# Optimization experiments

Hardware: AMD Instinct MI355X
Metric: run time of the kernel (lower is better)

Reference implementation:

```python
import jax, jax.numpy as jnp
import numpy as np

DIM = 1024
H = 16
HD = DIM // H  # 64
K = 256


def setup_inputs() -> dict:
    key = jax.random.key(0)
    ks = jax.random.split(key, 8)
    x = jax.random.normal(ks[0], (4, 4096, DIM), dtype=jnp.float32)
    # torch nn.Linear weights are (out, in); y = x @ W.T
    Wq = jax.random.normal(ks[1], (DIM, DIM), dtype=jnp.float32) * (DIM ** -0.5)
    Wk = jax.random.normal(ks[2], (DIM, DIM), dtype=jnp.float32) * (DIM ** -0.5)
    Wv = jax.random.normal(ks[3], (DIM, DIM), dtype=jnp.float32) * (DIM ** -0.5)
    E = jax.random.normal(ks[4], (K, HD), dtype=jnp.float32)
    F = jax.random.normal(ks[5], (K, HD), dtype=jnp.float32)
    Wo = jax.random.normal(ks[6], (DIM, DIM), dtype=jnp.float32) * (DIM ** -0.5)
    bo = jax.random.normal(ks[7], (DIM,), dtype=jnp.float32) * 0.01
    return {"x": x, "Wq": Wq, "Wk": Wk, "Wv": Wv, "E": E, "F": F, "Wo": Wo, "bo": bo}


def reference(x, Wq, Wk, Wv, E, F, Wo, bo):
    B, N, D = x.shape
    d = HD
    q = (x @ Wq.T).reshape(B, N, H, d).transpose(0, 2, 1, 3)  # (B,H,N,d)
    k = (x @ Wk.T).reshape(B, N, H, d).transpose(0, 2, 1, 3)
    v = (x @ Wv.T).reshape(B, N, H, d).transpose(0, 2, 1, 3)
    # Faithful to source: einsum contracts over n (sequence), elementwise in d.
    k_proj = jnp.einsum('bhnd,kd->bhkd', k, E)  # (B,H,K,d)
    v_proj = jnp.einsum('bhnd,kd->bhkd', v, F)
    attn = jnp.einsum('bhnd,bhkd->bhnk', q, k_proj) / (d ** 0.5)  # (B,H,N,K)
    attn = jax.nn.softmax(attn, axis=-1)
    out = jnp.einsum('bhnk,bhkd->bhnd', attn, v_proj)
    out = out.transpose(0, 2, 1, 3).reshape(B, N, D)
    return out @ Wo.T + bo
```

## Files before the change

### kernel.cpp

```cpp
#include <hip/hip_runtime.h>

#define DIM 1024
#define BATCH 4
#define SEQ 4096
#define NH 16
#define HD 64
#define KP 256

typedef float f32x4 __attribute__((ext_vector_type(4)));
typedef _Float16 half8 __attribute__((ext_vector_type(8)));

__device__ __forceinline__ void gll16(const void* g, void* l) {
  __builtin_amdgcn_global_load_lds(
      (const __attribute__((address_space(1))) void*)g,
      (__attribute__((address_space(3))) void*)l, 16, 0, 0);
}

#define DPPF(v, ctrl)                                                        \
  __builtin_bit_cast(float, __builtin_amdgcn_mov_dpp(                        \
                                __builtin_bit_cast(int, v), ctrl, 0xF, 0xF, true))

__global__ void k_cvt(const float* __restrict__ s, _Float16* __restrict__ d) {
  int i = (blockIdx.x * 256 + threadIdx.x) * 8;
  f32x4 a = *(const f32x4*)(s + i);
  f32x4 b = *(const f32x4*)(s + i + 4);
  half8 h;
  h[0] = a[0]; h[1] = a[1]; h[2] = a[2]; h[3] = a[3];
  h[4] = b[0]; h[5] = b[1]; h[6] = b[2]; h[7] = b[3];
  *(half8*)(d + i) = h;
}

__global__ void k_cvtw(const float* __restrict__ Wq, const float* __restrict__ Wo,
                       _Float16* __restrict__ Wq_h, _Float16* __restrict__ Wo_h) {
  int bb = blockIdx.x;
  const float* s = (bb < 512) ? Wq : Wo;
  _Float16* d = (bb < 512) ? Wq_h : Wo_h;
  int i = ((bb & 511) * 256 + threadIdx.x) * 8;
  f32x4 a = *(const f32x4*)(s + i);
  f32x4 b = *(const f32x4*)(s + i + 4);
  half8 h;
  h[0] = a[0]; h[1] = a[1]; h[2] = a[2]; h[3] = a[3];
  h[4] = b[0]; h[5] = b[1]; h[6] = b[2]; h[7] = b[3];
  *(half8*)(d + i) = h;
}

__global__ void k_misc(const float* __restrict__ E, const float* __restrict__ F,
                       _Float16* __restrict__ E_h, _Float16* __restrict__ Ft,
                       float* __restrict__ xsum) {
  int bb = blockIdx.x;
  if (bb < 16) {
    xsum[bb * 256 + threadIdx.x] = 0.f;
  } else if (bb < 24) {
    int i = ((bb - 16) * 256 + threadIdx.x) * 8;
    f32x4 a = *(const f32x4*)(E + i);
    f32x4 b = *(const f32x4*)(E + i + 4);
    half8 h;
    h[0] = a[0]; h[1] = a[1]; h[2] = a[2]; h[3] = a[3];
    h[4] = b[0]; h[5] = b[1]; h[6] = b[2]; h[7] = b[3];
    *(half8*)(E_h + i) = h;
  } else {
    int i = (bb - 24) * 256 + threadIdx.x;
    int k = i >> 6, d = i & 63;
    Ft[d * KP + (k & 15) * 16 + (k >> 4)] = (_Float16)F[i];
  }
}

__global__ void k_xsum(const _Float16* __restrict__ xh, float* __restrict__ xs) {
  int c = blockIdx.x * 256 + threadIdx.x;
  int b = blockIdx.y;
  int n0 = blockIdx.z * 128;
  const _Float16* p = xh + (size_t)(b * SEQ + n0) * DIM + c;
  float s = 0.f;
  #pragma unroll 8
  for (int i = 0; i < 128; i++) s += (float)p[i * DIM];
  atomicAdd(&xs[b * DIM + c], s);
}

__global__ void k_sksv(const float* __restrict__ xs, const float* __restrict__ Wk,
                       const float* __restrict__ Wv, float* __restrict__ Sk,
                       float* __restrict__ Sv) {
  int idx = blockIdx.x * 4 + (threadIdx.x >> 6);
  int lane = threadIdx.x & 63;
  int kv = idx >> 12;
  int rem = idx & 4095;
  int b = rem >> 10, c = rem & 1023;
  const float* W = (kv ? Wv : Wk) + c * DIM;
  const float* xp = xs + b * DIM;
  float a = 0.f;
  #pragma unroll
  for (int i = 0; i < 16; i++) a += xp[lane + i * 64] * W[lane + i * 64];
  for (int off = 32; off; off >>= 1) a += __shfl_down(a, off);
  if (lane == 0) (kv ? Sv : Sk)[rem] = a;
}

template <int MODE>
__global__ __launch_bounds__(512, 2) void k_gemm(const _Float16* __restrict__ A,
                                                 const _Float16* __restrict__ Bw,
                                                 void* __restrict__ Cout,
                                                 const float* __restrict__ sb) {
  __shared__ _Float16 sh[4][2][8192];
  const int tid = threadIdx.x;
  const int w = tid >> 6, l = tid & 63;
  const int q4 = l >> 4, mm = l & 15;
  const int wm = w & 1, wn = w >> 1;
  const int m0 = blockIdx.x * 256, n0 = blockIdx.y * 256;
  f32x4 acc[8][4] = {};

  const int schunk = ((l & 3) ^ ((l >> 3) & 3)) * 8;
  const _Float16* Ag = A + (size_t)(m0 + w * 32 + (l >> 2)) * DIM + schunk;
  const _Float16* Bg = Bw + (size_t)(n0 + w * 32 + (l >> 2)) * DIM + schunk;
  const int sdst = w * 1024;
  const int csw = (q4 ^ ((mm >> 1) & 3)) * 8;
  const int rdo_a = (wm * 128 + mm) * 32 + csw;
  const int rdo_b = (wn * 64 + mm) * 32 + csw;

  gll16(Ag, &sh[0][0][sdst]);
  gll16(Ag + 16 * DIM, &sh[0][0][sdst + 512]);
  gll16(Bg, &sh[0][1][sdst]);
  gll16(Bg + 16 * DIM, &sh[0][1][sdst + 512]);
  gll16(Ag + 32, &sh[1][0][sdst]);
  gll16(Ag + 32 + 16 * DIM, &sh[1][0][sdst + 512]);
  gll16(Bg + 32, &sh[1][1][sdst]);
  gll16(Bg + 32 + 16 * DIM, &sh[1][1][sdst + 512]);
  asm volatile("s_waitcnt vmcnt(4)" ::: "memory");
  __builtin_amdgcn_s_barrier();

  #pragma unroll 4
  for (int t = 0; t < 32; t++) {
    const int s = t & 3, rs = (t + 2) & 3;
    if (t < 30) {
      const int kn = (t + 2) * 32;
      gll16(Ag + kn, &sh[rs][0][sdst]);
      gll16(Ag + kn + 16 * DIM, &sh[rs][0][sdst + 512]);
      gll16(Bg + kn, &sh[rs][1][sdst]);
      gll16(Bg + kn + 16 * DIM, &sh[rs][1][sdst + 512]);
    }
    const _Float16* Ap = &sh[s][0][rdo_a];
    const _Float16* Bp = &sh[s][1][rdo_b];
    half8 bv[4], av[8];
    #pragma unroll
    for (int i = 0; i < 4; i++) bv[i] = *(const half8*)(Bp + i * 512);
    #pragma unroll
    for (int i = 0; i < 8; i++) av[i] = *(const half8*)(Ap + i * 512);
    __builtin_amdgcn_s_setprio(1);
    #pragma unroll
    for (int mt = 0; mt < 8; mt++)
      #pragma unroll
      for (int nt = 0; nt < 4; nt++)
        acc[mt][nt] = __builtin_amdgcn_mfma_f32_16x16x32_f16(av[mt], bv[nt], acc[mt][nt], 0, 0, 0);
    __builtin_amdgcn_s_setprio(0);
    if (t < 30) {
      asm volatile("s_waitcnt vmcnt(4)" ::: "memory");
    } else if (t == 30) {
      asm volatile("s_waitcnt vmcnt(0)" ::: "memory");
    }
    __builtin_amdgcn_s_barrier();
  }

  if (MODE == 0) {
    _Float16* Lh = (_Float16*)sh;
    const float lsc = 0.125f * 1.44269504088896f;
    #pragma unroll
    for (int p = 0; p < 4; p++) {
      if (wm == (p >> 1)) {
        #pragma unroll
        for (int nt = 0; nt < 4; nt++) {
          const int cl = wn * 64 + nt * 16 + mm;
          const float s = sb[(m0 >> 12) * DIM + n0 + cl] * lsc;
          #pragma unroll
          for (int mtl = 0; mtl < 4; mtl++) {
            const int mt = (p & 1) * 4 + mtl;
            const int rl = mtl * 16 + q4 * 4;
            #pragma unroll
            for (int r = 0; r < 4; r++)
              Lh[(rl + r) * 264 + cl] = (_Float16)(acc[mt][nt][r] * s);
          }
        }
      }
      __syncthreads();
      const int row_l = tid >> 3, c0 = (tid & 7) * 32;
      _Float16* dst = (_Float16*)Cout + (size_t)(m0 + p * 64 + row_l) * DIM + n0 + c0;
      #pragma unroll
      for (int i = 0; i < 4; i++)
        *(half8*)(dst + i * 8) = *(half8*)(Lh + row_l * 264 + c0 + i * 8);
      __syncthreads();
    }
  } else {
    float* Lf = (float*)sh;
    #pragma unroll
    for (int p = 0; p < 8; p++) {
      if (wm == (p >> 2)) {
        #pragma unroll
        for (int nt = 0; nt < 4; nt++) {
          const int cl = wn * 64 + nt * 16 + mm;
          const float s = sb[n0 + cl];
          #pragma unroll
          for (int mtl = 0; mtl < 2; mtl++) {
            const int mt = (p & 3) * 2 + mtl;
            const int rl = mtl * 16 + q4 * 4;
            #pragma unroll
            for (int r = 0; r < 4; r++)
              Lf[(rl + r) * 260 + cl] = acc[mt][nt][r] + s;
          }
        }
      }
      __syncthreads();
      const int row_l = tid >> 4, c0 = (tid & 15) * 16;
      float* dst = (float*)Cout + (size_t)(m0 + p * 32 + row_l) * DIM + n0 + c0;
      #pragma unroll
      for (int i = 0; i < 4; i++)
        *(f32x4*)(dst + i * 4) = *(f32x4*)(Lf + row_l * 260 + c0 + i * 4);
      __syncthreads();
    }
  }
}

__global__ __launch_bounds__(256) void k_attn(const _Float16* __restrict__ Q,
                                              const _Float16* __restrict__ E,
                                              const _Float16* __restrict__ Ftp,
                                              const float* __restrict__ Sv,
                                              _Float16* __restrict__ O) {
  __shared__ _Float16 Ps[4][16][264];
  const int tid = threadIdx.x;
  const int w = tid >> 6, lane = tid & 63;
  const int q4 = lane >> 4, mm = lane & 15;
  const int bh = blockIdx.y;
  const int b = bh >> 4, h = bh & 15;
  const int row_base = blockIdx.x * 512 + w * 128;

  half8 ef[16][2];
  #pragma unroll
  for (int t = 0; t < 16; t++)
    #pragma unroll
    for (int kk = 0; kk < 2; kk++)
      ef[t][kk] = *(const half8*)(E + (t * 16 + mm) * HD + kk * 32 + q4 * 8);
  half8 ff[4][8];
  #pragma unroll
  for (int nt = 0; nt < 4; nt++)
    #pragma unroll
    for (int kk = 0; kk < 8; kk++)
      ff[nt][kk] = *(const half8*)(Ftp + (nt * 16 + mm) * KP + kk * 32 + q4 * 8);
  float sv[4];
  #pragma unroll
  for (int nt = 0; nt < 4; nt++) sv[nt] = Sv[b * DIM + h * HD + nt * 16 + mm];

  const _Float16* Qbase = Q + ((size_t)(b * SEQ + row_base + mm)) * DIM + h * HD + q4 * 8;
  half8 qa0 = *(const half8*)(Qbase);
  half8 qa1 = *(const half8*)(Qbase + 32);

  for (int tile = 0; tile < 8; tile++) {
    f32x4 acc[16] = {};
    #pragma unroll
    for (int t = 0; t < 16; t++)
      acc[t] = __builtin_amdgcn_mfma_f32_16x16x32_f16(qa0, ef[t][0], acc[t], 0, 0, 0);
    #pragma unroll
    for (int t = 0; t < 16; t++)
      acc[t] = __builtin_amdgcn_mfma_f32_16x16x32_f16(qa1, ef[t][1], acc[t], 0, 0, 0);
    half8 qn0, qn1;
    if (tile < 7) {
      const _Float16* Qn = Qbase + (size_t)(tile + 1) * 16 * DIM;
      qn0 = *(const half8*)(Qn);
      qn1 = *(const half8*)(Qn + 32);
    }
    float mx[4] = {-1e30f, -1e30f, -1e30f, -1e30f};
    #pragma unroll
    for (int t = 0; t < 16; t++)
      #pragma unroll
      for (int r = 0; r < 4; r++) mx[r] = fmaxf(mx[r], acc[t][r]);
    #pragma unroll
    for (int r = 0; r < 4; r++) {
      float m = mx[r];
      m = fmaxf(m, DPPF(m, 0x121));
      m = fmaxf(m, DPPF(m, 0x122));
      m = fmaxf(m, DPPF(m, 0x124));
      m = fmaxf(m, DPPF(m, 0x128));
      mx[r] = m;
    }
    float sm[4] = {0.f, 0.f, 0.f, 0.f};
    #pragma unroll
    for (int t = 0; t < 16; t++)
      #pragma unroll
      for (int r = 0; r < 4; r++) {
        float p = __builtin_amdgcn_exp2f(acc[t][r] - mx[r]);
        acc[t][r] = p;
        sm[r] += p;
      }
    #pragma unroll
    for (int r = 0; r < 4; r++) {
      float s = sm[r];
      s += DPPF(s, 0x121);
      s += DPPF(s, 0x122);
      s += DPPF(s, 0x124);
      s += DPPF(s, 0x128);
      sm[r] = 1.f / s;
    }
    #pragma unroll
    for (int r = 0; r < 4; r++) {
      half8 h0, h1;
      #pragma unroll
      for (int t = 0; t < 8; t++) h0[t] = (_Float16)acc[t][r];
      #pragma unroll
      for (int t = 0; t < 8; t++) h1[t] = (_Float16)acc[t + 8][r];
      *(half8*)&Ps[w][q4 * 4 + r][mm * 16] = h0;
      *(half8*)&Ps[w][q4 * 4 + r][mm * 16 + 8] = h1;
    }
    f32x4 acc2[4] = {};
    #pragma unroll
    for (int kk = 0; kk < 8; kk++) {
      half8 pa = *(const half8*)&Ps[w][mm][kk * 32 + q4 * 8];
      #pragma unroll
      for (int nt = 0; nt < 4; nt++)
        acc2[nt] = __builtin_amdgcn_mfma_f32_16x16x32_f16(pa, ff[nt][kk], acc2[nt], 0, 0, 0);
    }
    const int rw0 = row_base + tile * 16;
    #pragma unroll
    for (int nt = 0; nt < 4; nt++)
      #pragma unroll
      for (int r = 0; r < 4; r++)
        O[(size_t)(b * SEQ + rw0 + q4 * 4 + r) * DIM + h * HD + nt * 16 + mm] =
            (_Float16)(acc2[nt][r] * (sm[r] * sv[nt]));
    qa0 = qn0;
    qa1 = qn1;
  }
}

extern "C" void kernel_launch(void* const* d_in, const int* in_sizes, int n_in,
                              void* d_out, int out_size, void* d_ws, size_t ws_size,
                              hipStream_t stream) {
  (void)in_sizes; (void)n_in; (void)out_size; (void)ws_size;
  const float* x  = (const float*)d_in[0];
  const float* Wq = (const float*)d_in[1];
  const float* Wk = (const float*)d_in[2];
  const float* Wv = (const float*)d_in[3];
  const float* E  = (const float*)d_in[4];
  const float* F  = (const float*)d_in[5];
  const float* Wo = (const float*)d_in[6];
  const float* bo = (const float*)d_in[7];
  char* ws = (char*)d_ws;
  _Float16* x_h  = (_Float16*)(ws);
  _Float16* O_h  = (_Float16*)(ws);
  _Float16* Q_h  = (_Float16*)(ws + 33554432);
  _Float16* Wq_h = (_Float16*)(ws + 67108864);
  _Float16* Wo_h = (_Float16*)(ws + 69206016);
  _Float16* E_h  = (_Float16*)(ws + 71303168);
  _Float16* Ft_h = (_Float16*)(ws + 71335936);
  float* xsum    = (float*)(ws + 71368704);
  float* Sk      = (float*)(ws + 71385088);
  float* Sv      = (float*)(ws + 71401472);
  float* out     = (float*)d_out;

  k_cvt<<<8192, 256, 0, stream>>>(x, x_h);
  k_misc<<<88, 256, 0, stream>>>(E, F, E_h, Ft_h, xsum);
  k_cvtw<<<1024, 256, 0, stream>>>(Wq, Wo, Wq_h, Wo_h);
  k_xsum<<<dim3(4, BATCH, 32), 256, 0, stream>>>(x_h, xsum);
  k_sksv<<<2048, 256, 0, stream>>>(xsum, Wk, Wv, Sk, Sv);
  k_gemm<0><<<dim3(64, 4), 512, 0, stream>>>(x_h, Wq_h, (void*)Q_h, Sk);
  k_attn<<<dim3(8, 64), 256, 0, stream>>>(Q_h, E_h, Ft_h, Sv, O_h);
  k_gemm<1><<<dim3(64, 4), 512, 0, stream>>>(O_h, Wo_h, (void*)out, bo);
}
```

Before: 299.3 us.

## Restructure GEMM main loop into double-buffered 64-wide K tiles with phased loads

Replaces the 4-stage, 32-wide K pipeline with a double-buffered 64-wide K tile, split into four phases. Each phase issues explicit ds_read_b128 fragment loads, then a global-to-LDS prefetch of the next tile, then an MFMA burst under barriers. It also remaps block indices with a swizzle to improve L2 reuse across neighbouring tiles. The aim is to interleave LDS reads, global prefetch and MFMA more tightly, and to cut loop overhead. The cost is many more barriers and hand-written inline asm with manual waitcnt management, which is fragile.

```diff
diff --git a/kernel.cpp b/kernel.cpp
--- a/kernel.cpp
+++ b/kernel.cpp
@@ -9,12 +9,28 @@
 
 typedef float f32x4 __attribute__((ext_vector_type(4)));
 typedef _Float16 half8 __attribute__((ext_vector_type(8)));
+typedef int i32x4 __attribute__((ext_vector_type(4)));
 
 __device__ __forceinline__ void gll16(const void* g, void* l) {
   __builtin_amdgcn_global_load_lds(
       (const __attribute__((address_space(1))) void*)g,
       (__attribute__((address_space(3))) void*)l, 16, 0, 0);
 }
+
+__device__ __forceinline__ unsigned lds_addr(const void* p) {
+  return (unsigned)(size_t)(const __attribute__((address_space(3))) void*)p;
+}
+
+#define DSR128(dst, base, imm)                                               \
+  asm volatile("ds_read_b128 %0, %1 offset:" #imm : "=&v"(dst) : "v"(base))
+
+#define BARR __builtin_amdgcn_s_barrier()
+#define LGKM0                                                                \
+  do {                                                                       \
+    asm volatile("s_waitcnt lgkmcnt(0)" ::: "memory");                       \
+    __builtin_amdgcn_sched_barrier(0);                                       \
+  } while (0)
+#define VMC(n) asm volatile("s_waitcnt vmcnt(" #n ")" ::: "memory")
 
 #define DPPF(v, ctrl)                                                        \
   __builtin_bit_cast(float, __builtin_amdgcn_mov_dpp(                        \
@@ -93,68 +109,110 @@
   if (lane == 0) (kv ? Sv : Sk)[rem] = a;
 }
 
+#define MF(X, Y, C)                                                          \
+  __builtin_amdgcn_mfma_f32_16x16x32_f16(__builtin_bit_cast(half8, (X)),     \
+                                         __builtin_bit_cast(half8, (Y)),     \
+                                         (C), 0, 0, 0)
+#define MFROW(AI, FA)                                                        \
+  acc[AI][0] = MF(FA, fb[0], acc[AI][0]);                                    \
+  acc[AI][1] = MF(FA, fb[1], acc[AI][1]);                                    \
+  acc[AI][2] = MF(FA, fb[2], acc[AI][2]);                                    \
+  acc[AI][3] = MF(FA, fb[3], acc[AI][3]);
+
+#define STG(GP, DB, MAT, H, TT)                                              \
+  do {                                                                       \
+    gll16((GP) + (TT) * 64 + (H) * 32,                                       \
+          shp + (DB) * 32768 + (MAT) * 16384 + (H) * 8192 + wofs);           \
+    gll16((GP) + 131072 + (TT) * 64 + (H) * 32,                              \
+          shp + (DB) * 32768 + (MAT) * 16384 + (H) * 8192 + 4096 + wofs);    \
+  } while (0)
+
+#define TILE(T, AL, BL, XD, STEN, VM2Z, P4VM)                                \
+  {                                                                          \
+    i32x4 fa[4], fb[4];                                                      \
+                      \
+    DSR128(fb[0], BL, 32768); DSR128(fb[1], BL, 33792);                      \
+    DSR128(fb[2], BL, 34816); DSR128(fb[3], BL, 35840);                      \
+    DSR128(fa[0], AL, 0);     DSR128(fa[1], AL, 1024);                       \
+    DSR128(fa[2], AL, 2048);  DSR128(fa[3], AL, 3072);                       \
+    if (STEN) { STG(Agp, XD, 0, 0, (T) + 1); }                               \
+    BARR; LGKM0;                                                             \
+    __builtin_amdgcn_s_setprio(1);                                           \
+    MFROW(0, fa[0]) MFROW(1, fa[1]) MFROW(2, fa[2]) MFROW(3, fa[3])          \
+    __builtin_amdgcn_s_setprio(0);                                           \
+    BARR;                                                                    \
+                             \
+    DSR128(fa[0], AL, 4096);  DSR128(fa[1], AL, 5120);                       \
+    DSR128(fa[2], AL, 6144);  DSR128(fa[3], AL, 7168);                       \
+    if (STEN) { STG(Bgp, XD, 1, 0, (T) + 1); }                               \
+    BARR; LGKM0;                                                             \
+    __builtin_amdgcn_s_setprio(1);                                           \
+    MFROW(4, fa[0]) MFROW(5, fa[1]) MFROW(6, fa[2]) MFROW(7, fa[3])          \
+    __builtin_amdgcn_s_setprio(0);                                           \
+    if (VM2Z) { VMC(0); } else { VMC(4); }                                   \
+    BARR;                                                                    \
+                      \
+    DSR128(fb[0], BL, 49152); DSR128(fb[1], BL, 50176);                      \
+    DSR128(fb[2], BL, 51200); DSR128(fb[3], BL, 52224);                      \
+    DSR128(fa[0], AL, 16384); DSR128(fa[1], AL, 17408);                      \
+    DSR128(fa[2], AL, 18432); DSR128(fa[3], AL, 19456);                      \
+    if (STEN) { STG(Agp, XD, 0, 1, (T) + 1); }                               \
+    BARR; LGKM0;                                                             \
+    __builtin_amdgcn_s_setprio(1);                                           \
+    MFROW(0, fa[0]) MFROW(1, fa[1]) MFROW(2, fa[2]) MFROW(3, fa[3])          \
+    __builtin_amdgcn_s_setprio(0);                                           \
+    BARR;                                                                    \
+                             \
+    DSR128(fa[0], AL, 20480); DSR128(fa[1], AL, 21504);                      \
+    DSR128(fa[2], AL, 22528); DSR128(fa[3], AL, 23552);                      \
+    if (STEN) { STG(Bgp, XD, 1, 1, (T) + 1); }                               \
+    BARR; LGKM0;                                                             \
+    __builtin_amdgcn_s_setprio(1);                                           \
+    MFROW(4, fa[0]) MFROW(5, fa[1]) MFROW(6, fa[2]) MFROW(7, fa[3])          \
+    __builtin_amdgcn_s_setprio(0);                                           \
+    if (P4VM) { VMC(4); }                                                    \
+    BARR;                                                                    \
+  }
+
 template <int MODE>
 __global__ __launch_bounds__(512, 2) void k_gemm(const _Float16* __restrict__ A,
                                                  const _Float16* __restrict__ Bw,
                                                  void* __restrict__ Cout,
                                                  const float* __restrict__ sb) {
-  __shared__ _Float16 sh[4][2][8192];
+  __shared__ _Float16 sh[65536];
   const int tid = threadIdx.x;
   const int w = tid >> 6, l = tid & 63;
   const int q4 = l >> 4, mm = l & 15;
   const int wm = w & 1, wn = w >> 1;
-  const int m0 = blockIdx.x * 256, n0 = blockIdx.y * 256;
+  const int lin = blockIdx.y * 64 + blockIdx.x;
+  const int sw = (lin & 7) * 32 + (lin >> 3);
+  const int m0 = (sw & 63) * 256, n0 = (sw >> 6) * 256;
   f32x4 acc[8][4] = {};
 
-  const int schunk = ((l & 3) ^ ((l >> 3) & 3)) * 8;
-  const _Float16* Ag = A + (size_t)(m0 + w * 32 + (l >> 2)) * DIM + schunk;
-  const _Float16* Bg = Bw + (size_t)(n0 + w * 32 + (l >> 2)) * DIM + schunk;
-  const int sdst = w * 1024;
-  const int csw = (q4 ^ ((mm >> 1) & 3)) * 8;
-  const int rdo_a = (wm * 128 + mm) * 32 + csw;
-  const int rdo_b = (wn * 64 + mm) * 32 + csw;
-
-  gll16(Ag, &sh[0][0][sdst]);
-  gll16(Ag + 16 * DIM, &sh[0][0][sdst + 512]);
-  gll16(Bg, &sh[0][1][sdst]);
-  gll16(Bg + 16 * DIM, &sh[0][1][sdst + 512]);
-  gll16(Ag + 32, &sh[1][0][sdst]);
-  gll16(Ag + 32 + 16 * DIM, &sh[1][0][sdst + 512]);
-  gll16(Bg + 32, &sh[1][1][sdst]);
-  gll16(Bg + 32 + 16 * DIM, &sh[1][1][sdst + 512]);
-  asm volatile("s_waitcnt vmcnt(4)" ::: "memory");
-  __builtin_amdgcn_s_barrier();
-
-  #pragma unroll 4
-  for (int t = 0; t < 32; t++) {
-    const int s = t & 3, rs = (t + 2) & 3;
-    if (t < 30) {
-      const int kn = (t + 2) * 32;
-      gll16(Ag + kn, &sh[rs][0][sdst]);
-      gll16(Ag + kn + 16 * DIM, &sh[rs][0][sdst + 512]);
-      gll16(Bg + kn, &sh[rs][1][sdst]);
-      gll16(Bg + kn + 16 * DIM, &sh[rs][1][sdst + 512]);
-    }
-    const _Float16* Ap = &sh[s][0][rdo_a];
-    const _Float16* Bp = &sh[s][1][rdo_b];
-    half8 bv[4], av[8];
-    #pragma unroll
-    for (int i = 0; i < 4; i++) bv[i] = *(const half8*)(Bp + i * 512);
-    #pragma unroll
-    for (int i = 0; i < 8; i++) av[i] = *(const half8*)(Ap + i * 512);
-    __builtin_amdgcn_s_setprio(1);
-    #pragma unroll
-    for (int mt = 0; mt < 8; mt++)
-      #pragma unroll
-      for (int nt = 0; nt < 4; nt++)
-        acc[mt][nt] = __builtin_amdgcn_mfma_f32_16x16x32_f16(av[mt], bv[nt], acc[mt][nt], 0, 0, 0);
-    __builtin_amdgcn_s_setprio(0);
-    if (t < 30) {
-      asm volatile("s_waitcnt vmcnt(4)" ::: "memory");
-    } else if (t == 30) {
-      asm volatile("s_waitcnt vmcnt(0)" ::: "memory");
-    }
-    __builtin_amdgcn_s_barrier();
+  const int sch8 = ((l & 3) ^ ((l >> 3) & 3)) * 8;
+  const _Float16* Agp = A + (size_t)(m0 + w * 16 + (l >> 2)) * DIM + sch8;
+  const _Float16* Bgp = Bw + (size_t)(n0 + w * 16 + (l >> 2)) * DIM + sch8;
+  _Float16* shp = sh;
+  const int wofs = w * 512;
+
+  const int sw16 = (q4 ^ ((mm >> 1) & 3)) * 16;
+  const unsigned shb = lds_addr(sh);
+  const unsigned aL0 = shb + (unsigned)((wm * 128 + mm) * 64 + sw16);
+  const unsigned aL1 = aL0 + 65536u;
+  const unsigned bL0 = shb + (unsigned)((wn * 64 + mm) * 64 + sw16);
+  const unsigned bL1 = bL0 + 65536u;
+
+  STG(Agp, 0, 0, 0, -1 + 1);
+  STG(Bgp, 0, 1, 0, 0);
+  STG(Agp, 0, 0, 1, 0);
+  STG(Bgp, 0, 1, 1, 0);
+  VMC(0);
+  BARR;
+
+  for (int tp = 0; tp < 8; tp++) {
+    TILE(2 * tp, aL0, bL0, 1, 1, 0, 1);
+    const int st = (tp < 7);
+    TILE(2 * tp + 1, aL1, bL1, 0, st, !st, st);
   }
 
   if (MODE == 0) {
```

New measurement: 308.6 us. +3.1%, slower.

## Replace direct global-to-LDS 4-stage pipeline with register-staged double buffering

Applied to the files above, without the earlier changes.

The GEMM main loop no longer uses global_load_lds into a 4-deep LDS ring. It loads the next K-slice into registers, runs the MFMAs on the current LDS buffer, then writes the registers into the other of two LDS buffers behind a barrier. This halves LDS use and lets the XOR swizzle be applied on the LDS write side. In exchange it costs extra VGPRs and LDS store instructions, and prefetch depth drops from two stages to one, which may expose more memory latency.

```diff
diff --git a/kernel.cpp b/kernel.cpp
--- a/kernel.cpp
+++ b/kernel.cpp
@@ -9,12 +9,6 @@
 
 typedef float f32x4 __attribute__((ext_vector_type(4)));
 typedef _Float16 half8 __attribute__((ext_vector_type(8)));
-
-__device__ __forceinline__ void gll16(const void* g, void* l) {
-  __builtin_amdgcn_global_load_lds(
-      (const __attribute__((address_space(1))) void*)g,
-      (__attribute__((address_space(3))) void*)l, 16, 0, 0);
-}
 
 #define DPPF(v, ctrl)                                                        \
   __builtin_bit_cast(float, __builtin_amdgcn_mov_dpp(                        \
@@ -98,7 +92,7 @@
                                                  const _Float16* __restrict__ Bw,
                                                  void* __restrict__ Cout,
                                                  const float* __restrict__ sb) {
-  __shared__ _Float16 sh[4][2][8192];
+  __shared__ _Float16 sh[2][2][8192];
   const int tid = threadIdx.x;
   const int w = tid >> 6, l = tid & 63;
   const int q4 = l >> 4, mm = l & 15;
@@ -106,38 +100,38 @@
   const int m0 = blockIdx.x * 256, n0 = blockIdx.y * 256;
   f32x4 acc[8][4] = {};
 
-  const int schunk = ((l & 3) ^ ((l >> 3) & 3)) * 8;
-  const _Float16* Ag = A + (size_t)(m0 + w * 32 + (l >> 2)) * DIM + schunk;
-  const _Float16* Bg = Bw + (size_t)(n0 + w * 32 + (l >> 2)) * DIM + schunk;
-  const int sdst = w * 1024;
+  const int rowl = w * 32 + (l >> 2);
+  const _Float16* Ag = A + (size_t)(m0 + rowl) * DIM + (l & 3) * 8;
+  const _Float16* Bg = Bw + (size_t)(n0 + rowl) * DIM + (l & 3) * 8;
+  const int wofs = rowl * 32 + ((l & 3) ^ ((l >> 3) & 3)) * 8;
   const int csw = (q4 ^ ((mm >> 1) & 3)) * 8;
   const int rdo_a = (wm * 128 + mm) * 32 + csw;
   const int rdo_b = (wn * 64 + mm) * 32 + csw;
 
-  gll16(Ag, &sh[0][0][sdst]);
-  gll16(Ag + 16 * DIM, &sh[0][0][sdst + 512]);
-  gll16(Bg, &sh[0][1][sdst]);
-  gll16(Bg + 16 * DIM, &sh[0][1][sdst + 512]);
-  gll16(Ag + 32, &sh[1][0][sdst]);
-  gll16(Ag + 32 + 16 * DIM, &sh[1][0][sdst + 512]);
-  gll16(Bg + 32, &sh[1][1][sdst]);
-  gll16(Bg + 32 + 16 * DIM, &sh[1][1][sdst + 512]);
-  asm volatile("s_waitcnt vmcnt(4)" ::: "memory");
-  __builtin_amdgcn_s_barrier();
-
-  #pragma unroll 4
+  half8 ra0, ra1, rb0, rb1;
+  ra0 = *(const half8*)(Ag);
+  ra1 = *(const half8*)(Ag + 16 * DIM);
+  rb0 = *(const half8*)(Bg);
+  rb1 = *(const half8*)(Bg + 16 * DIM);
+  *(half8*)&sh[0][0][wofs] = ra0;
+  *(half8*)&sh[0][0][wofs + 512] = ra1;
+  *(half8*)&sh[0][1][wofs] = rb0;
+  *(half8*)&sh[0][1][wofs + 512] = rb1;
+  __syncthreads();
+
+  #pragma unroll 2
   for (int t = 0; t < 32; t++) {
-    const int s = t & 3, rs = (t + 2) & 3;
-    if (t < 30) {
-      const int kn = (t + 2) * 32;
-      gll16(Ag + kn, &sh[rs][0][sdst]);
-      gll16(Ag + kn + 16 * DIM, &sh[rs][0][sdst + 512]);
-      gll16(Bg + kn, &sh[rs][1][sdst]);
-      gll16(Bg + kn + 16 * DIM, &sh[rs][1][sdst + 512]);
-    }
-    const _Float16* Ap = &sh[s][0][rdo_a];
-    const _Float16* Bp = &sh[s][1][rdo_b];
-    half8 bv[4], av[8];
+    const int cur = t & 1;
+    if (t < 31) {
+      const int kn = (t + 1) * 32;
+      ra0 = *(const half8*)(Ag + kn);
+      ra1 = *(const half8*)(Ag + kn + 16 * DIM);
+      rb0 = *(const half8*)(Bg + kn);
+      rb1 = *(const half8*)(Bg + kn + 16 * DIM);
+    }
+    half8 av[8], bv[4];
+    const _Float16* Ap = &sh[cur][0][rdo_a];
+    const _Float16* Bp = &sh[cur][1][rdo_b];
     #pragma unroll
     for (int i = 0; i < 4; i++) bv[i] = *(const half8*)(Bp + i * 512);
     #pragma unroll
@@ -149,12 +143,16 @@
       for (int nt = 0; nt < 4; nt++)
         acc[mt][nt] = __builtin_amdgcn_mfma_f32_16x16x32_f16(av[mt], bv[nt], acc[mt][nt], 0, 0, 0);
     __builtin_amdgcn_s_setprio(0);
-    if (t < 30) {
-      asm volatile("s_waitcnt vmcnt(4)" ::: "memory");
-    } else if (t == 30) {
-      asm volatile("s_waitcnt vmcnt(0)" ::: "memory");
-    }
-    __builtin_amdgcn_s_barrier();
+    __builtin_amdgcn_sched_barrier(0);
+    if (t < 31) {
+      _Float16* dA = &sh[cur ^ 1][0][wofs];
+      _Float16* dB = &sh[cur ^ 1][1][wofs];
+      *(half8*)dA = ra0;
+      *(half8*)(dA + 512) = ra1;
+      *(half8*)dB = rb0;
+      *(half8*)(dB + 512) = rb1;
+    }
+    __syncthreads();
   }
 
   if (MODE == 0) {
```

Result: no change. 301.4 us (+0.7%).
